# Kernel optimization log

Hardware: AMD Instinct MI355X
Metric: run time of the kernel (lower is better)

## Reference

```python
import jax, jax.numpy as jnp
import numpy as np

D_MODEL = 1024
STATE_DIM = 256
BATCH = 4
SEQ_LEN = 4096


def setup_inputs() -> dict:
    key = jax.random.key(0)
    k_u, k_B, k_C = jax.random.split(key, 3)
    u = jax.random.normal(k_u, (BATCH, SEQ_LEN, D_MODEL), dtype=jnp.float32)
    # parameters (as in torch init)
    log_lambda = jnp.linspace(2.94, 4.6, STATE_DIM, dtype=jnp.float32)
    # nn.Linear weight shape is [out_features, in_features]
    B_w = jax.random.normal(k_B, (STATE_DIM, D_MODEL), dtype=jnp.float32) / np.sqrt(D_MODEL)
    C_w = jax.random.normal(k_C, (D_MODEL, STATE_DIM), dtype=jnp.float32) / np.sqrt(STATE_DIM)
    D = jnp.ones((D_MODEL,), dtype=jnp.float32)
    return {"u": u, "log_lambda": log_lambda, "B_w": B_w, "C_w": C_w, "D": D}


def reference(u, log_lambda, B_w, C_w, D):
    batch, seq_len, d = u.shape
    # Bu = B(u): [B, L, N]
    Bu = jnp.einsum("bld,nd->bln", u, B_w)
    lam = jax.nn.sigmoid(log_lambda)                     # [N]
    t = jnp.arange(seq_len, dtype=lam.dtype)
    kernel = lam[None, :] ** t[:, None]                  # [L, N]
    # next power of two >= 2*L (static)
    fft_len = 1
    while fft_len < 2 * seq_len:
        fft_len *= 2
    K_hat = jnp.fft.rfft(kernel, n=fft_len, axis=0)      # [F, N]
    Bu_hat = jnp.fft.rfft(Bu, n=fft_len, axis=1)         # [B, F, N]
    h_hat = K_hat[None, :, :] * Bu_hat
    h = jnp.fft.irfft(h_hat, n=fft_len, axis=1)[:, :seq_len, :]  # [B, L, N]
    y = jnp.einsum("bln,dn->bld", h, C_w) + D * u
    return y
```

## Files before the change

kernel.cpp:

```cpp
#include <hip/hip_runtime.h>
#include <hip/hip_bf16.h>

#define D_MODEL 1024
#define STATE_N 256
#define BATCH 4
#define SEQ_LEN 4096
#define M_TOTAL (BATCH * SEQ_LEN)
#define NCHUNK 128
#define CHUNK (SEQ_LEN / NCHUNK)

typedef __attribute__((ext_vector_type(8))) short bf16x8;
typedef __attribute__((ext_vector_type(4))) short s16x4;
typedef __attribute__((ext_vector_type(2))) short s16x2;
typedef __attribute__((ext_vector_type(4))) float f32x4;

static __device__ inline short f2bf(float f) {
    union { float f; unsigned u; } v; v.f = f;
    unsigned r = v.u + 0x7FFFu + ((v.u >> 16) & 1u);
    return (short)(r >> 16);
}
static __device__ inline short f2bf_hw(float f) {
    __hip_bfloat16 h = __float2bfloat16(f);
    return *reinterpret_cast<const short*>(&h);
}
static __device__ inline float bf2f(short s) {
    union { unsigned u; float f; } v;
    v.u = ((unsigned)(unsigned short)s) << 16;
    return v.f;
}
static __device__ inline float sigmoidf(float x) { return 1.0f / (1.0f + expf(-x)); }

#define GLOAD_LDS16(gp, lp)                                                     \
    __builtin_amdgcn_global_load_lds(                                           \
        (const __attribute__((address_space(1))) void*)(gp),                    \
        (__attribute__((address_space(3))) void*)(lp), 16, 0, 0)

#define WAITVM0   asm volatile("s_waitcnt vmcnt(0)" ::: "memory")
#define WAITVM4   asm volatile("s_waitcnt vmcnt(4)" ::: "memory")
#define WAITLGKM0 asm volatile("s_waitcnt lgkmcnt(0)" ::: "memory")
#define BARRIER() do { __builtin_amdgcn_s_barrier(); asm volatile("" ::: "memory"); } while (0)

__global__ void prep(const float* __restrict__ Bw, const float* __restrict__ Cw,
                     const float* __restrict__ ll,
                     short* __restrict__ Bwt, short* __restrict__ Cwt,
                     float* __restrict__ W) {
    const int bx = blockIdx.x, tid = threadIdx.x;
    if (bx >= 256) {
        const int i = bx - 256, n = tid;
        W[i * 256 + n] = powf(sigmoidf(ll[n]), (float)(31 - i));
        return;
    }
    const int g = bx * 256 + tid;
    const float* s; short* d;
    if (g < 32768) {
        const int col = g & 127, kc = (g >> 7) & 3, kt = (g >> 9) & 31, cb = g >> 14;
        s = Bw + (size_t)(cb * 128 + col) * D_MODEL + kt * 32 + kc * 8;
        d = Bwt + (size_t)g * 8;
    } else {
        const int h = g - 32768;
        const int col = h & 63, ksq = (h >> 6) & 7, tt = (h >> 9) & 3, cb = h >> 11;
        s = Cw + (size_t)(cb * 64 + col) * STATE_N + tt * 64 + ksq * 8;
        d = Cwt + (size_t)h * 8;
    }
    const f32x4 v0 = *(const f32x4*)s;
    const f32x4 v1 = *(const f32x4*)(s + 4);
    bf16x8 r;
    #pragma unroll
    for (int q = 0; q < 4; ++q) { r[q] = f2bf(v0[q]); r[4 + q] = f2bf(v1[q]); }
    *(bf16x8*)d = r;
}

__global__ __launch_bounds__(256, 3) void gemm1(const float* __restrict__ u,
                                                const short* __restrict__ Bwt,
                                                const float* __restrict__ W,
                                                short* __restrict__ Bu,
                                                float* __restrict__ ends) {
    __shared__ float As[3][64 * 32];
    __shared__ short Bs[3][4 * 128 * 8];
    const int tid = threadIdx.x;
    const int lane = tid & 63, wave = tid >> 6;
    const int lr = lane & 15, kq = lane >> 4;
    const int wr = wave >> 1, wc = wave & 1;
    const int wg = ((blockIdx.x & 7) << 6) + (blockIdx.x >> 3);
    const int cb = wg & 1, strip = wg >> 1;
    const int m0 = strip * 64, n0 = cb * 128;

    const int r0 = tid >> 3, gx = tid & 7;
    const int sw0 = r0 & 7;
    const float* asrc0 = u + (size_t)(m0 + r0) * D_MODEL + ((gx ^ sw0) << 2);
    const float* asrc1 = u + (size_t)(m0 + 32 + r0) * D_MODEL + ((gx ^ sw0) << 2);
    const short* bsrc = Bwt + (size_t)cb * 32 * 4096;

    #define STAGE1(BUF, KT)                                                      \
        do { GLOAD_LDS16(asrc0 + (KT) * 32, (char*)&As[BUF][0] + (wave * 64) * 16);        \
             GLOAD_LDS16(asrc1 + (KT) * 32, (char*)&As[BUF][0] + (256 + wave * 64) * 16);  \
             const short* bs_ = bsrc + (size_t)(KT) * 4096;                      \
             GLOAD_LDS16(bs_ + (size_t)tid * 8,       (char*)&Bs[BUF][0] + (wave * 64) * 16);       \
             GLOAD_LDS16(bs_ + (size_t)(256 + tid) * 8, (char*)&Bs[BUF][0] + (256 + wave * 64) * 16); \
        } while (0)

    f32x4 acc[2][4] = {};

    STAGE1(0, 0);
    STAGE1(1, 1);

    #pragma unroll
    for (int t = 0; t < 32; ++t) {
        if (t < 31) { WAITVM4; } else { WAITVM0; }
        BARRIER();
        if (t + 2 <= 31) STAGE1((t + 2) % 3, t + 2);

        bf16x8 af[2];
        bf16x8 bfr[4];
        #pragma unroll
        for (int i = 0; i < 2; ++i) {
            const int row = wr * 32 + i * 16 + lr;
            const int sw = row & 7;
            const f32x4 a0 = *(const f32x4*)&As[t % 3][row * 32 + ((((kq << 1)    ) ^ sw) << 2)];
            const f32x4 a1 = *(const f32x4*)&As[t % 3][row * 32 + ((((kq << 1) | 1) ^ sw) << 2)];
            #pragma unroll
            for (int e = 0; e < 4; ++e) { af[i][e] = f2bf_hw(a0[e]); af[i][4 + e] = f2bf_hw(a1[e]); }
        }
        #pragma unroll
        for (int j = 0; j < 4; ++j)
            bfr[j] = *(const bf16x8*)&Bs[t % 3][(kq * 128 + wc * 64 + j * 16 + lr) * 8];
        #pragma unroll
        for (int i = 0; i < 2; ++i)
            #pragma unroll
            for (int j = 0; j < 4; ++j)
                acc[i][j] = __builtin_amdgcn_mfma_f32_16x16x32_bf16(bfr[j], af[i], acc[i][j], 0, 0, 0);
    }
    #undef STAGE1

    #pragma unroll
    for (int i = 0; i < 2; ++i) {
        const int m = m0 + wr * 32 + i * 16 + lr;
        #pragma unroll
        for (int j = 0; j < 4; ++j) {
            const int n = n0 + wc * 64 + j * 16 + kq * 4;
            s16x4 st;
            #pragma unroll
            for (int r = 0; r < 4; ++r) st[r] = f2bf(acc[i][j][r]);
            *(s16x4*)(Bu + (size_t)m * STATE_N + n) = st;
        }
    }

    float part[4][4];
    #pragma unroll
    for (int j = 0; j < 4; ++j) {
        const int nb = n0 + wc * 64 + j * 16 + kq * 4;
        const f32x4 w0 = *(const f32x4*)(W + (size_t)lr * 256 + nb);
        const f32x4 w1 = *(const f32x4*)(W + (size_t)(16 + lr) * 256 + nb);
        #pragma unroll
        for (int r = 0; r < 4; ++r)
            part[j][r] = w0[r] * acc[0][j][r] + w1[r] * acc[1][j][r];
    }
    #pragma unroll
    for (int m = 1; m <= 8; m <<= 1)
        #pragma unroll
        for (int j = 0; j < 4; ++j)
            #pragma unroll
            for (int r = 0; r < 4; ++r)
                part[j][r] += __shfl_xor(part[j][r], m, 64);
    if (lr == 0) {
        const int cg = strip * 2 + wr;
        #pragma unroll
        for (int j = 0; j < 4; ++j) {
            f32x4 e;
            #pragma unroll
            for (int r = 0; r < 4; ++r) e[r] = part[j][r];
            *(f32x4*)(ends + (size_t)cg * STATE_N + n0 + wc * 64 + j * 16 + kq * 4) = e;
        }
    }
}

__global__ __launch_bounds__(256, 2) void gemm2(const short* __restrict__ Bu,
                                                const short* __restrict__ Cwt,
                                                const float* __restrict__ ll,
                                                const float* __restrict__ carries,
                                                const float* __restrict__ u,
                                                const float* __restrict__ Dv,
                                                float* __restrict__ y) {
    __shared__ short Ash[4][64 * 64];
    const int tid = threadIdx.x;
    const int lane = tid & 63, wave = tid >> 6;
    const int lr = lane & 15, kq = lane >> 4;
    const int wg = ((blockIdx.x & 7) << 7) + (blockIdx.x >> 3);
    const int cb = wg & 3, strip = wg >> 2;
    const int m0 = strip * 64;

    const int ch = tid >> 7;
    const int cp = tid & 127;
    const int st = cp >> 5;
    const int c0 = (2 * cp) & 63;
    const int scc = c0 >> 3, scw = c0 & 7;

    const float2 lraw = *(const float2*)(ll + 2 * cp);
    const float2 car2 = *(const float2*)(carries + (size_t)(strip * 2 + ch) * STATE_N + 2 * cp);

    const int aslot0 = wave * 128 + lane, aslot1 = aslot0 + 64;
    const int arow0 = aslot0 >> 3, arow1 = aslot1 >> 3;
    const int ac = lane & 7;
    const short* ag0 = Bu + (size_t)(m0 + arow0) * STATE_N + ((ac ^ (arow0 & 7)) << 3);
    const short* ag1 = Bu + (size_t)(m0 + arow1) * STATE_N + ((ac ^ (arow1 & 7)) << 3);
    const short* bg = Cwt + (size_t)(cb * 4 + wave) * 16384;

    #pragma unroll
    for (int t = 0; t < 4; ++t) {
        GLOAD_LDS16(ag0 + t * 64, (char*)&Ash[t][0] + aslot0 * 16);
        GLOAD_LDS16(ag1 + t * 64, (char*)&Ash[t][0] + aslot1 * 16);
    }
    WAITVM0;
    BARRIER();

    bf16x8 bfr[2][2][4];
    #define LOADB2(BUF, T)                                                       \
        do { _Pragma("unroll")                                                   \
             for (int ks = 0; ks < 2; ++ks)                                      \
                 _Pragma("unroll")                                               \
                 for (int j = 0; j < 4; ++j)                                     \
                     bfr[BUF][ks][j] = *(const bf16x8*)(bg + (size_t)(T) * 4096  \
                         + (((ks << 2) | kq) * 64 + j * 16 + lr) * 8); } while (0)

    LOADB2(0, 0);

    {
        const float lam0 = sigmoidf(lraw.x), lam1 = sigmoidf(lraw.y);
        s16x2 rv[32];
        #pragma unroll
        for (int i = 0; i < 32; ++i)
            rv[i] = *(const s16x2*)&Ash[st][(ch * 32 + i) * 64 + ((scc ^ (i & 7)) << 3) + scw];
        float h0 = car2.x, h1 = car2.y;
        #pragma unroll
        for (int i = 0; i < 32; ++i) {
            h0 = fmaf(lam0, h0, bf2f(rv[i][0]));
            h1 = fmaf(lam1, h1, bf2f(rv[i][1]));
            s16x2 o; o[0] = f2bf_hw(h0); o[1] = f2bf_hw(h1);
            rv[i] = o;
        }
        #pragma unroll
        for (int i = 0; i < 32; ++i)
            *(s16x2*)&Ash[st][(ch * 32 + i) * 64 + ((scc ^ (i & 7)) << 3) + scw] = rv[i];
    }
    WAITLGKM0;
    BARRIER();

    f32x4 acc[4][4] = {};
    #pragma unroll
    for (int t = 0; t < 4; ++t) {
        bf16x8 af[2][4];
        #pragma unroll
        for (int ks = 0; ks < 2; ++ks)
            #pragma unroll
            for (int i = 0; i < 4; ++i) {
                const int row = i * 16 + lr;
                af[ks][i] = *(const bf16x8*)&Ash[t][row * 64 + ((((ks << 2) | kq) ^ (row & 7)) << 3)];
            }
        if (t < 3) LOADB2((t + 1) & 1, t + 1);
        #pragma unroll
        for (int ks = 0; ks < 2; ++ks)
            #pragma unroll
            for (int i = 0; i < 4; ++i)
                #pragma unroll
                for (int j = 0; j < 4; ++j)
                    acc[i][j] = __builtin_amdgcn_mfma_f32_16x16x32_bf16(bfr[t & 1][ks][j], af[ks][i], acc[i][j], 0, 0, 0);
    }
    #undef LOADB2

    #pragma unroll
    for (int i = 0; i < 4; ++i) {
        const int m = m0 + i * 16 + lr;
        #pragma unroll
        for (int j = 0; j < 4; ++j) {
            const int n = cb * 256 + wave * 64 + j * 16 + kq * 4;
            const size_t o = (size_t)m * D_MODEL + n;
            const f32x4 uv = *(const f32x4*)(u + o);
            const f32x4 dv = *(const f32x4*)(Dv + n);
            f32x4 rv;
            #pragma unroll
            for (int q = 0; q < 4; ++q) rv[q] = fmaf(dv[q], uv[q], acc[i][j][q]);
            *(f32x4*)(y + o) = rv;
        }
    }
}

__global__ void scan_carry(const float* __restrict__ ends,
                           const float* __restrict__ log_lambda,
                           float* __restrict__ carries) {
    const int n = threadIdx.x;
    const int b = blockIdx.x;
    const float lam = sigmoidf(log_lambda[n]);
    const float lamC = powf(lam, (float)CHUNK);
    float carry = 0.0f;
    #pragma unroll 16
    for (int c = 0; c < NCHUNK; ++c) {
        const size_t o = ((size_t)(b * NCHUNK + c)) * STATE_N + n;
        carries[o] = carry;
        carry = fmaf(lamC, carry, ends[o]);
    }
}

extern "C" void kernel_launch(void* const* d_in, const int* in_sizes, int n_in,
                              void* d_out, int out_size, void* d_ws, size_t ws_size,
                              hipStream_t stream) {
    const float* u  = (const float*)d_in[0];
    const float* ll = (const float*)d_in[1];
    const float* Bw = (const float*)d_in[2];
    const float* Cw = (const float*)d_in[3];
    const float* Dv = (const float*)d_in[4];
    float* y = (float*)d_out;

    char* ws = (char*)d_ws;
    size_t off = 0;
    short* Bwt = (short*)(ws + off); off += (size_t)STATE_N * D_MODEL * 2;
    short* Cwt = (short*)(ws + off); off += (size_t)D_MODEL * STATE_N * 2;
    float* W   = (float*)(ws + off); off += (size_t)32 * STATE_N * 4;
    short* Bu  = (short*)(ws + off); off += (size_t)M_TOTAL * STATE_N * 2;
    float* ends = (float*)(ws + off); off += (size_t)BATCH * NCHUNK * STATE_N * 4;
    float* carries = (float*)(ws + off);

    prep<<<288, 256, 0, stream>>>(Bw, Cw, ll, Bwt, Cwt, W);
    gemm1<<<512, 256, 0, stream>>>(u, Bwt, W, Bu, ends);
    scan_carry<<<BATCH, STATE_N, 0, stream>>>(ends, ll, carries);
    gemm2<<<1024, 256, 0, stream>>>(Bu, Cwt, ll, carries, u, Dv, y);
}
```

Baseline: 66.26 us.

## Halve gemm2 row tile to 32 and scan one state per thread

Shrinks the gemm2 row strip from 64 to 32 rows, so the grid doubles to 2048 blocks. Each of the 256 threads now does the in-LDS chunk scan for one state dimension over 32 rows, working directly on LDS instead of register-buffered pairs. The LDS tile becomes a single 32x256 swizzled layout and launch bounds rise to 3 blocks per CU. The goal is more parallelism and occupancy and a shorter scan per block, at the cost of loading the Cw tile twice as often per output row and lower MFMA reuse. It also relies on carries now being produced per 32-row chunk, which needs the other kernels to match.

```diff
diff --git a/kernel.cpp b/kernel.cpp
--- a/kernel.cpp
+++ b/kernel.cpp
@@ -174,41 +174,32 @@
     }
 }
 
-__global__ __launch_bounds__(256, 2) void gemm2(const short* __restrict__ Bu,
+__global__ __launch_bounds__(256, 3) void gemm2(const short* __restrict__ Bu,
                                                 const short* __restrict__ Cwt,
                                                 const float* __restrict__ ll,
                                                 const float* __restrict__ carries,
                                                 const float* __restrict__ u,
                                                 const float* __restrict__ Dv,
                                                 float* __restrict__ y) {
-    __shared__ short Ash[4][64 * 64];
+    __shared__ short Ash[32 * 256];
     const int tid = threadIdx.x;
     const int lane = tid & 63, wave = tid >> 6;
     const int lr = lane & 15, kq = lane >> 4;
-    const int wg = ((blockIdx.x & 7) << 7) + (blockIdx.x >> 3);
+    const int wg = ((blockIdx.x & 7) << 8) + (blockIdx.x >> 3);
     const int cb = wg & 3, strip = wg >> 2;
-    const int m0 = strip * 64;
-
-    const int ch = tid >> 7;
-    const int cp = tid & 127;
-    const int st = cp >> 5;
-    const int c0 = (2 * cp) & 63;
-    const int scc = c0 >> 3, scw = c0 & 7;
-
-    const float2 lraw = *(const float2*)(ll + 2 * cp);
-    const float2 car2 = *(const float2*)(carries + (size_t)(strip * 2 + ch) * STATE_N + 2 * cp);
-
-    const int aslot0 = wave * 128 + lane, aslot1 = aslot0 + 64;
-    const int arow0 = aslot0 >> 3, arow1 = aslot1 >> 3;
-    const int ac = lane & 7;
-    const short* ag0 = Bu + (size_t)(m0 + arow0) * STATE_N + ((ac ^ (arow0 & 7)) << 3);
-    const short* ag1 = Bu + (size_t)(m0 + arow1) * STATE_N + ((ac ^ (arow1 & 7)) << 3);
+    const int m0 = strip * 32;
+
+    const float lam = sigmoidf(ll[tid]);
+    float h = carries[(size_t)strip * STATE_N + tid];
+
+    const int arow = tid >> 5, ap = tid & 31;
     const short* bg = Cwt + (size_t)(cb * 4 + wave) * 16384;
 
     #pragma unroll
-    for (int t = 0; t < 4; ++t) {
-        GLOAD_LDS16(ag0 + t * 64, (char*)&Ash[t][0] + aslot0 * 16);
-        GLOAD_LDS16(ag1 + t * 64, (char*)&Ash[t][0] + aslot1 * 16);
+    for (int q = 0; q < 4; ++q) {
+        const int row = q * 8 + arow;
+        const short* src = Bu + (size_t)(m0 + row) * STATE_N + ((ap ^ (row & 7)) << 3);
+        GLOAD_LDS16(src, (char*)&Ash[0] + (q * 256 + wave * 64) * 16);
     }
     WAITVM0;
     BARRIER();
@@ -225,42 +216,34 @@
     LOADB2(0, 0);
 
     {
-        const float lam0 = sigmoidf(lraw.x), lam1 = sigmoidf(lraw.y);
-        s16x2 rv[32];
-        #pragma unroll
-        for (int i = 0; i < 32; ++i)
-            rv[i] = *(const s16x2*)&Ash[st][(ch * 32 + i) * 64 + ((scc ^ (i & 7)) << 3) + scw];
-        float h0 = car2.x, h1 = car2.y;
+        const int g = tid >> 3, s = tid & 7;
         #pragma unroll
         for (int i = 0; i < 32; ++i) {
-            h0 = fmaf(lam0, h0, bf2f(rv[i][0]));
-            h1 = fmaf(lam1, h1, bf2f(rv[i][1]));
-            s16x2 o; o[0] = f2bf_hw(h0); o[1] = f2bf_hw(h1);
-            rv[i] = o;
-        }
-        #pragma unroll
-        for (int i = 0; i < 32; ++i)
-            *(s16x2*)&Ash[st][(ch * 32 + i) * 64 + ((scc ^ (i & 7)) << 3) + scw] = rv[i];
+            const int a = (i * 32 + (g ^ (i & 7))) * 8 + s;
+            h = fmaf(lam, h, bf2f(Ash[a]));
+            Ash[a] = f2bf_hw(h);
+        }
     }
     WAITLGKM0;
     BARRIER();
 
-    f32x4 acc[4][4] = {};
+    f32x4 acc[2][4] = {};
     #pragma unroll
     for (int t = 0; t < 4; ++t) {
-        bf16x8 af[2][4];
+        bf16x8 af[2][2];
         #pragma unroll
         for (int ks = 0; ks < 2; ++ks)
             #pragma unroll
-            for (int i = 0; i < 4; ++i) {
+            for (int i = 0; i < 2; ++i) {
                 const int row = i * 16 + lr;
-                af[ks][i] = *(const bf16x8*)&Ash[t][row * 64 + ((((ks << 2) | kq) ^ (row & 7)) << 3)];
+                const int gk = t * 8 + ks * 4 + kq;
+                af[ks][i] = *(const bf16x8*)&Ash[(row * 32 + (gk ^ (row & 7))) * 8];
             }
         if (t < 3) LOADB2((t + 1) & 1, t + 1);
         #pragma unroll
         for (int ks = 0; ks < 2; ++ks)
             #pragma unroll
-            for (int i = 0; i < 4; ++i)
+            for (int i = 0; i < 2; ++i)
                 #pragma unroll
                 for (int j = 0; j < 4; ++j)
                     acc[i][j] = __builtin_amdgcn_mfma_f32_16x16x32_bf16(bfr[t & 1][ks][j], af[ks][i], acc[i][j], 0, 0, 0);
@@ -268,7 +251,7 @@
     #undef LOADB2
 
     #pragma unroll
-    for (int i = 0; i < 4; ++i) {
+    for (int i = 0; i < 2; ++i) {
         const int m = m0 + i * 16 + lr;
         #pragma unroll
         for (int j = 0; j < 4; ++j) {
@@ -322,5 +305,5 @@
     prep<<<288, 256, 0, stream>>>(Bw, Cw, ll, Bwt, Cwt, W);
     gemm1<<<512, 256, 0, stream>>>(u, Bwt, W, Bu, ends);
     scan_carry<<<BATCH, STATE_N, 0, stream>>>(ends, ll, carries);
-    gemm2<<<1024, 256, 0, stream>>>(Bu, Cwt, ll, carries, u, Dv, y);
-}
+    gemm2<<<2048, 256, 0, stream>>>(Bu, Cwt, ll, carries, u, Dv, y);
+}
```

New measurement: 66.26 us. About the same (+0.0%).
